# Kernel tuning notes

Measured on AMD Instinct MI355X. Metric: run time of the kernel, lower is better.

The kernel has to match this reference:

```python
import jax, jax.numpy as jnp
import numpy as np

F = 32          # conf['num_features']
G = 96          # voxel grid extent
N_VOX = 80000   # occupied input voxels
BN_EPS = 1e-5


def _encode(c):
    c = c.astype(np.int64) + 8
    return (c[:, 0] * 512 + c[:, 1]) * 512 + c[:, 2]


def _offsets(ks, dil):
    r = np.arange(-(ks // 2), ks // 2 + 1) * dil
    return np.stack(np.meshgrid(r, r, r, indexing='ij'), -1).reshape(-1, 3)


def _build_map(in_coords, out_coords, offsets):
    # For each kernel offset k and output voxel j, find input voxel index at
    # out_coords[j] + offsets[k]; sentinel = n_in / n_out when absent.
    n_in, n_out = len(in_coords), len(out_coords)
    keys = _encode(in_coords)
    order = np.argsort(keys).astype(np.int32)
    skeys = keys[order]
    K = len(offsets)
    in_map = np.full((K, n_out), n_in, np.int32)
    out_map = np.full((K, n_out), n_out, np.int32)
    base = np.arange(n_out, dtype=np.int32)
    for k, off in enumerate(offsets):
        q = _encode(out_coords + off)
        pos = np.clip(np.searchsorted(skeys, q), 0, n_in - 1)
        valid = skeys[pos] == q
        in_map[k] = np.where(valid, order[pos], n_in)
        out_map[k] = np.where(valid, base, n_out)
    return jnp.asarray(in_map), jnp.asarray(out_map)


def setup_inputs() -> dict:
    rng = np.random.default_rng(0)
    idx = rng.choice(G ** 3, size=N_VOX, replace=False)
    coords = np.stack(np.unravel_index(idx, (G, G, G)), 1).astype(np.int64)
    c2 = np.unique(coords // 2 * 2, axis=0)   # stride-2 coords (enc1 output)
    c4 = np.unique(coords // 4 * 4, axis=0)   # stride-4 coords (c_out.C)

    m1_in, m1_out = _build_map(coords, c2, _offsets(5, 1))  # k5 s2 conv
    m2_in, m2_out = _build_map(c2, c2, _offsets(3, 2))      # enc1 blocks
    m3_in, m3_out = _build_map(c2, c4, _offsets(3, 2))      # conv2 -> c_out.C
    m4_in, m4_out = _build_map(c4, c4, _offsets(3, 4))      # enc2 blocks

    key = jax.random.key(0)
    ks = jax.random.split(key, 8)
    s = 0.05
    return {
        'x_geo': jax.random.normal(ks[0], (N_VOX, 1), jnp.float32),
        'x_col': jax.random.uniform(ks[1], (N_VOX, 3), jnp.float32),
        'w0': jax.random.normal(ks[2], (125, 4, F), jnp.float32) * s,
        'w_e1': jax.random.normal(ks[3], (2, 2, 27, F, F), jnp.float32) * s,
        'g_e1': jnp.ones((2, 2, F), jnp.float32),
        'b_e1': jnp.zeros((2, 2, F), jnp.float32),
        'w2': jax.random.normal(ks[4], (27, F, 2 * F), jnp.float32) * s,
        'w_e2': jax.random.normal(ks[5], (2, 2, 27, 2 * F, 2 * F), jnp.float32) * s,
        'g_e2': jnp.ones((2, 2, 2 * F), jnp.float32),
        'b_e2': jnp.zeros((2, 2, 2 * F), jnp.float32),
        'm1_in': m1_in, 'm1_out': m1_out,
        'm2_in': m2_in, 'm2_out': m2_out,
        'm3_in': m3_in, 'm3_out': m3_out,
        'm4_in': m4_in, 'm4_out': m4_out,
    }


def sparse_conv(feats, W, in_map, out_map):
    # gather -> GEMM -> scatter per kernel offset (lax.scan over K offsets)
    n_out = out_map.shape[1]
    fpad = jnp.concatenate([feats, jnp.zeros((1, feats.shape[1]), feats.dtype)], 0)
    out0 = jnp.zeros((n_out + 1, W.shape[2]), feats.dtype)
    def step(acc, kmw):
        im, om, w = kmw
        return acc.at[om].add(fpad[im] @ w), None
    out, _ = jax.lax.scan(step, out0, (in_map, out_map, W))
    return out[:n_out]


def batch_norm(x, g, b):
    mu = x.mean(0)
    var = ((x - mu) ** 2).mean(0)
    return (x - mu) * jax.lax.rsqrt(var + BN_EPS) * g + b


def basic_block(x, w, g, b, in_map, out_map):
    # ME BasicBlock: conv-BN-ReLU-conv-BN + residual, ReLU
    y = jax.nn.relu(batch_norm(sparse_conv(x, w[0], in_map, out_map), g[0], b[0]))
    y = batch_norm(sparse_conv(y, w[1], in_map, out_map), g[1], b[1])
    return jax.nn.relu(y + x)


def reference(x_geo, x_col, w0, w_e1, g_e1, b_e1, w2, w_e2, g_e2, b_e2,
              m1_in, m1_out, m2_in, m2_out, m3_in, m3_out, m4_in, m4_out):
    x = jnp.concatenate([x_geo, x_col], axis=1)          # ME.cat -> 4 channels
    x = jax.nn.relu(sparse_conv(x, w0, m1_in, m1_out))   # k5 s2 conv + ReLU
    for i in range(2):                                   # enc1 residual blocks
        x = basic_block(x, w_e1[i], g_e1[i], b_e1[i], m2_in, m2_out)
    x = sparse_conv(x, w2, m3_in, m3_out)                # conv2 onto c_out.C
    for i in range(2):                                   # enc2 residual blocks
        x = basic_block(x, w_e2[i], g_e2[i], b_e2[i], m4_in, m4_out)
    return x
```

## Files before the change

kernel.cpp:

```cpp
#include <hip/hip_runtime.h>
#include <hip/hip_bf16.h>


typedef float f4 __attribute__((ext_vector_type(4)));
typedef short short8 __attribute__((ext_vector_type(8)));
typedef short short4v __attribute__((ext_vector_type(4)));

#define BN_EPS 1e-5f

static inline int ceil_div(int a, int b) { return (a + b - 1) / b; }

static __device__ inline float btof(short s) {
    unsigned u = ((unsigned)(unsigned short)s) << 16;
    float f;
    __builtin_memcpy(&f, &u, 4);
    return f;
}
static __device__ inline short ftob(float f) {
    __hip_bfloat16 h = __float2bfloat16(f);
    short s;
    __builtin_memcpy(&s, &h, 2);
    return s;
}

struct Seg {
    const float* W;
    long long begin, end;
    int K, CIN, COUT;
};

struct ProArgs {
    Seg s[10];
    const float* geo;
    const float* col;
    __hip_bfloat16* x0;
    int n_vox;
    float* stats;
    __hip_bfloat16* pads[5];
    int padn[5];
    long long wf_total;
    long long pro_total;
    __hip_bfloat16* Wf;
    const int* m1;
    __hip_bfloat16* A;
    int nc2;
};

template <int C>
__device__ inline void bn_coef(const float* st, const float* g, const float* b,
                               int c, int n, float& sc, float& sh) {
    float rn = 1.f / (float)n;
    float sum = st[c] + st[2 * C + c] + st[4 * C + c] + st[6 * C + c];
    float sq  = st[C + c] + st[3 * C + c] + st[5 * C + c] + st[7 * C + c];
    float mu = sum * rn;
    float inv = rsqrtf(sq * rn - mu * mu + BN_EPS);
    sc = inv * g[c];
    sh = b[c] - mu * sc;
}

__global__ __launch_bounds__(256) void k_prologue(ProArgs pa) {
    for (long long e = (long long)blockIdx.x * 256 + threadIdx.x; e < pa.pro_total;
         e += (long long)gridDim.x * 256) {
        if (e < pa.wf_total) {
            int si = 0;
#pragma unroll
            for (int i = 0; i < 10; ++i)
                if (e >= pa.s[i].end) si = i + 1;
            const Seg sg = pa.s[si];
            long long r = e - sg.begin;
            int j = (int)(r & 7);
            int lane = (int)((r >> 3) & 63);
            long long rest = r >> 9;
            int NT = sg.COUT >> 4;
            int ntile = (int)(rest % NT);
            int chunk = (int)(rest / NT);
            int kd = chunk * 32 + ((lane >> 4) << 3) + j;
            int koff = kd / sg.CIN;
            int ci = kd % sg.CIN;
            int n = ntile * 16 + (lane & 15);
            float v = (koff < sg.K) ? sg.W[((size_t)koff * sg.CIN + ci) * sg.COUT + n] : 0.f;
            pa.Wf[e] = __float2bfloat16(v);
            continue;
        }
        long long r = e - pa.wf_total;
        if (r < pa.n_vox) {
            int row = (int)r;
            pa.x0[row * 4 + 0] = __float2bfloat16(pa.geo[row]);
            pa.x0[row * 4 + 1] = __float2bfloat16(pa.col[row * 3 + 0]);
            pa.x0[row * 4 + 2] = __float2bfloat16(pa.col[row * 3 + 1]);
            pa.x0[row * 4 + 3] = __float2bfloat16(pa.col[row * 3 + 2]);
            continue;
        }
        r -= pa.n_vox;
        if (r < 4096) {
            pa.stats[r] = 0.f;
            continue;
        }
        r -= 4096;
#pragma unroll
        for (int i = 0; i < 5; ++i) {
            if (r < pa.padn[i]) {
                pa.pads[i][r] = __float2bfloat16(0.f);
                r = -1;
                break;
            }
            r -= pa.padn[i];
        }
    }
}

__global__ __launch_bounds__(256) void k_stem(ProArgs a) {
    const int t = threadIdx.x, w = t >> 6, lane = t & 63;
    const int quad = lane >> 4, ml = lane & 15;
    const int ntile = w & 1, mgroup = w >> 1;
    const int n_out = a.nc2, n_in = a.n_vox;
    const __hip_bfloat16* feat = a.x0;
    const __hip_bfloat16* Wf = a.Wf;
    const int* in_map = a.m1;
    __hip_bfloat16* out = a.A;
    const int mb = blockIdx.x * 64 + mgroup * 32;
    const int m0 = mb + ml, m1 = mb + 16 + ml;
    const bool v0 = m0 < n_out, v1 = m1 < n_out;
    f4 acc0 = {0.f, 0.f, 0.f, 0.f};
    f4 acc1 = {0.f, 0.f, 0.f, 0.f};
#pragma unroll 2
    for (int chunk = 0; chunk < 16; ++chunk) {
        int k0 = chunk * 8 + quad * 2;
        int k1 = k0 + 1;
        int k0c = (k0 < 125) ? k0 : 0;
        int k1c = (k1 < 125) ? k1 : 0;
        short8 b = *(const short8*)(Wf + ((size_t)(chunk * 2 + ntile) * 64 + lane) * 8);
        int ia = v0 ? in_map[(size_t)k0c * n_out + m0] : n_in;
        int ib = v0 ? in_map[(size_t)k1c * n_out + m0] : n_in;
        int ic = v1 ? in_map[(size_t)k0c * n_out + m1] : n_in;
        int id = v1 ? in_map[(size_t)k1c * n_out + m1] : n_in;
        short4v p0 = *(const short4v*)(feat + (size_t)ia * 4);
        short4v p1 = *(const short4v*)(feat + (size_t)ib * 4);
        short4v p2 = *(const short4v*)(feat + (size_t)ic * 4);
        short4v p3 = *(const short4v*)(feat + (size_t)id * 4);
        short8 a0, a1;
        a0[0] = p0[0]; a0[1] = p0[1]; a0[2] = p0[2]; a0[3] = p0[3];
        a0[4] = p1[0]; a0[5] = p1[1]; a0[6] = p1[2]; a0[7] = p1[3];
        a1[0] = p2[0]; a1[1] = p2[1]; a1[2] = p2[2]; a1[3] = p2[3];
        a1[4] = p3[0]; a1[5] = p3[1]; a1[6] = p3[2]; a1[7] = p3[3];
        acc0 = __builtin_amdgcn_mfma_f32_16x16x32_bf16(a0, b, acc0, 0, 0, 0);
        acc1 = __builtin_amdgcn_mfma_f32_16x16x32_bf16(a1, b, acc1, 0, 0, 0);
    }
    const int col = ntile * 16 + ml;
#pragma unroll
    for (int i = 0; i < 4; ++i) {
        int r0 = mb + quad * 4 + i;
        if (r0 < n_out)
            out[(size_t)r0 * 32 + col] = __float2bfloat16(fmaxf(acc0[i], 0.f));
        int r1 = mb + 16 + quad * 4 + i;
        if (r1 < n_out)
            out[(size_t)r1 * 32 + col] = __float2bfloat16(fmaxf(acc1[i], 0.f));
    }
}

template <int CIN, int COUT, int MT, int K, bool BNF>
__global__ __launch_bounds__(256, 4) void k_conv(
    const __hip_bfloat16* __restrict__ feat,
    const __hip_bfloat16* __restrict__ Wf,
    const int* __restrict__ in_map,
    __hip_bfloat16* __restrict__ out,
    float* __restrict__ stats,
    const float* __restrict__ in_stats,
    const float* __restrict__ in_g,
    const float* __restrict__ in_b,
    int n_out, int n_in) {
    constexpr int NT = COUT / 16;
    constexpr int H = CIN / 32;
    constexpr int R = MT * 16;
    constexpr int KPW = (K + 3) / 4;
    constexpr int SP = COUT + 1;
    const int t = threadIdx.x, w = t >> 6, lane = t & 63;
    const int quad = lane >> 4, ml = lane & 15;
    const int mb = blockIdx.x * R;

    __shared__ float red[4 * R * SP];
    __shared__ float sred[2 * 256];
    __shared__ float ibn[2 * CIN];

    if constexpr (BNF) {
        if (t < CIN) {
            float sc, sh;
            bn_coef<CIN>(in_stats, in_g, in_b, t, n_in, sc, sh);
            ibn[t] = sc;
            ibn[CIN + t] = sh;
        }
        __syncthreads();
    }
    float scr[H][8], shr[H][8];
    if constexpr (BNF) {
#pragma unroll
        for (int h = 0; h < H; ++h)
#pragma unroll
            for (int j = 0; j < 8; ++j) {
                int ch = h * 32 + quad * 8 + j;
                scr[h][j] = ibn[ch];
                shr[h][j] = ibn[CIN + ch];
            }
    }

    f4 acc[MT * NT];
#pragma unroll
    for (int i = 0; i < MT * NT; ++i) acc[i] = (f4){0.f, 0.f, 0.f, 0.f};

#pragma unroll
    for (int kk = 0; kk < KPW; ++kk) {
        const int k = kk * 4 + w;
        const int krow = (k < K) ? k : 0;
        const int* mk = in_map + (size_t)krow * n_out;
        int idx[MT];
#pragma unroll
        for (int mi = 0; mi < MT; ++mi) {
            int m = mb + mi * 16 + ml;
            idx[mi] = (m < n_out) ? mk[m] : n_in;
        }
        short8 bfrag[H * NT];
#pragma unroll
        for (int h = 0; h < H; ++h)
#pragma unroll
            for (int nt = 0; nt < NT; ++nt)
                bfrag[h * NT + nt] = *(const short8*)(
                    Wf + (((size_t)(k * H + h) * NT + nt) * 64 + lane) * 8);
#pragma unroll
        for (int mi = 0; mi < MT; ++mi) {
            const __hip_bfloat16* fp = feat + (size_t)idx[mi] * CIN + quad * 8;
            const bool sent = (idx[mi] == n_in);
#pragma unroll
            for (int h = 0; h < H; ++h) {
                short8 av = *(const short8*)(fp + h * 32);
                if constexpr (BNF) {
#pragma unroll
                    for (int j = 0; j < 8; ++j) {
                        float f = btof(av[j]) * scr[h][j] + shr[h][j];
                        f = fmaxf(f, 0.f);
                        av[j] = sent ? (short)0 : ftob(f);
                    }
                }
#pragma unroll
                for (int nt = 0; nt < NT; ++nt)
                    acc[mi * NT + nt] = __builtin_amdgcn_mfma_f32_16x16x32_bf16(
                        av, bfrag[h * NT + nt], acc[mi * NT + nt], 0, 0, 0);
            }
        }
    }

#pragma unroll
    for (int mi = 0; mi < MT; ++mi)
#pragma unroll
        for (int nt = 0; nt < NT; ++nt)
#pragma unroll
            for (int i = 0; i < 4; ++i)
                red[((size_t)w * R + mi * 16 + quad * 4 + i) * SP + nt * 16 + ml] =
                    acc[mi * NT + nt][i];
    __syncthreads();

    constexpr int E = (R * COUT) / 256;
    constexpr int RSTEP = 256 / COUT;
    const int col = t % COUT;
    const int rg = t / COUT;
    float s = 0.f, s2 = 0.f;
#pragma unroll
    for (int i = 0; i < E; ++i) {
        int r = rg + i * RSTEP;
        float v = red[(0 * R + r) * SP + col] + red[(1 * R + r) * SP + col] +
                  red[(2 * R + r) * SP + col] + red[(3 * R + r) * SP + col];
        s += v;
        s2 += v * v;
        int grow = mb + r;
        if (grow < n_out) out[(size_t)grow * COUT + col] = __float2bfloat16(v);
    }

    if (stats) {
        sred[t] = s;
        sred[256 + t] = s2;
        __syncthreads();
        if (t < 2 * COUT) {
            int c = t % COUT;
            int which = t / COUT;
            float v = 0.f;
#pragma unroll
            for (int j = 0; j < RSTEP; ++j) v += sred[which * 256 + j * COUT + c];
            atomicAdd(&stats[((blockIdx.x & 3) * 2 + which) * COUT + c], v);
        }
    }
}

template <int C, bool F32OUT>
__global__ __launch_bounds__(256) void k_bnres(
    const __hip_bfloat16* __restrict__ y, const __hip_bfloat16* __restrict__ res,
    const float* __restrict__ st, const float* __restrict__ g,
    const float* __restrict__ b, void* outp, int n) {
    __shared__ float ibn[2 * C];
    const int t = threadIdx.x;
    if (t < C) {
        float sc, sh;
        bn_coef<C>(st, g, b, t, n, sc, sh);
        ibn[t] = sc;
        ibn[C + t] = sh;
    }
    __syncthreads();
    long long tot = (long long)n * (C / 8);
    long long i = (long long)blockIdx.x * 256 + t;
    if (i >= tot) return;
    int c0 = (int)(i % (C / 8)) * 8;
    short8 v = *(const short8*)(y + i * 8);
    short8 r = *(const short8*)(res + i * 8);
    if constexpr (F32OUT) {
        float* out = (float*)outp;
        f4 o0, o1;
#pragma unroll
        for (int j = 0; j < 8; ++j) {
            float f = btof(v[j]) * ibn[c0 + j] + ibn[C + c0 + j] + btof(r[j]);
            f = fmaxf(f, 0.f);
            if (j < 4) o0[j] = f; else o1[j - 4] = f;
        }
        *(f4*)(out + i * 8) = o0;
        *(f4*)(out + i * 8 + 4) = o1;
    } else {
        __hip_bfloat16* out = (__hip_bfloat16*)outp;
        short8 o;
#pragma unroll
        for (int j = 0; j < 8; ++j) {
            float f = btof(v[j]) * ibn[c0 + j] + ibn[C + c0 + j] + btof(r[j]);
            o[j] = ftob(fmaxf(f, 0.f));
        }
        *(short8*)(out + i * 8) = o;
    }
}

extern "C" void kernel_launch(void* const* d_in, const int* in_sizes, int n_in_cnt,
                              void* d_out, int out_size, void* d_ws, size_t ws_size,
                              hipStream_t stream) {
    const float* x_geo = (const float*)d_in[0];
    const float* x_col = (const float*)d_in[1];
    const float* w0    = (const float*)d_in[2];
    const float* w_e1  = (const float*)d_in[3];
    const float* g_e1  = (const float*)d_in[4];
    const float* b_e1  = (const float*)d_in[5];
    const float* w2    = (const float*)d_in[6];
    const float* w_e2  = (const float*)d_in[7];
    const float* g_e2  = (const float*)d_in[8];
    const float* b_e2  = (const float*)d_in[9];
    const int* m1 = (const int*)d_in[10];
    const int* m2 = (const int*)d_in[12];
    const int* m3 = (const int*)d_in[14];
    const int* m4 = (const int*)d_in[16];

    const int n_vox = in_sizes[0];
    const int nc2 = in_sizes[10] / 125;
    const int nc4 = in_sizes[14] / 27;
    (void)out_size; (void)ws_size; (void)n_in_cnt;

    char* p = (char*)d_ws;
    auto alloc = [&](size_t bytes) -> char* {
        char* r = p;
        p += (bytes + 255) & ~(size_t)255;
        return r;
    };
    float* stats = (float*)alloc(8 * 512 * sizeof(float));
    __hip_bfloat16* x0 = (__hip_bfloat16*)alloc((size_t)(n_vox + 1) * 4 * 2);
    __hip_bfloat16* A  = (__hip_bfloat16*)alloc((size_t)(nc2 + 1) * 32 * 2);
    __hip_bfloat16* B  = (__hip_bfloat16*)alloc((size_t)(nc2 + 1) * 32 * 2);
    __hip_bfloat16* Cb = (__hip_bfloat16*)alloc((size_t)(nc2 + 1) * 32 * 2);
    __hip_bfloat16* D  = (__hip_bfloat16*)alloc((size_t)(nc4 + 1) * 64 * 2);
    __hip_bfloat16* E  = (__hip_bfloat16*)alloc((size_t)(nc4 + 1) * 64 * 2);
    __hip_bfloat16* Fb = (__hip_bfloat16*)alloc((size_t)(nc4 + 1) * 64 * 2);

    const long long sz_stem = 16LL * 2 * 512;
    const long long sz_e1   = 28LL * 2 * 512;
    const long long sz_c2   = 28LL * 4 * 512;
    const long long sz_e2   = 56LL * 4 * 512;
    const long long wf_total = sz_stem + 4 * sz_e1 + sz_c2 + 4 * sz_e2;
    __hip_bfloat16* Wf = (__hip_bfloat16*)alloc((size_t)wf_total * 2);

    ProArgs pa;
    long long cur = 0;
    auto seg = [&](int i, const float* W, int K, int CIN, int COUT, long long n) {
        pa.s[i].W = W; pa.s[i].K = K; pa.s[i].CIN = CIN; pa.s[i].COUT = COUT;
        pa.s[i].begin = cur; pa.s[i].end = cur + n; cur += n;
    };
    seg(0, w0, 125, 4, 32, sz_stem);
    for (int i = 0; i < 4; ++i)
        seg(1 + i, w_e1 + (size_t)i * 27 * 32 * 32, 27, 32, 32, sz_e1);
    seg(5, w2, 27, 32, 64, sz_c2);
    for (int i = 0; i < 4; ++i)
        seg(6 + i, w_e2 + (size_t)i * 27 * 64 * 64, 27, 64, 64, sz_e2);

    long long off_e1[4], off_e2[4];
    cur = sz_stem;
    for (int i = 0; i < 4; ++i) { off_e1[i] = cur; cur += sz_e1; }
    long long off_c2 = cur; cur += sz_c2;
    for (int i = 0; i < 4; ++i) { off_e2[i] = cur; cur += sz_e2; }

    pa.geo = x_geo; pa.col = x_col; pa.x0 = x0; pa.n_vox = n_vox;
    pa.stats = stats;
    pa.pads[0] = x0 + (size_t)n_vox * 4; pa.padn[0] = 4;
    pa.pads[1] = A + (size_t)nc2 * 32;   pa.padn[1] = 32;
    pa.pads[2] = B + (size_t)nc2 * 32;   pa.padn[2] = 32;
    pa.pads[3] = D + (size_t)nc4 * 64;   pa.padn[3] = 64;
    pa.pads[4] = E + (size_t)nc4 * 64;   pa.padn[4] = 64;
    pa.wf_total = wf_total;
    pa.pro_total = wf_total + n_vox + 4096 + (4 + 32 + 32 + 64 + 64);
    pa.Wf = Wf;
    pa.m1 = m1;
    pa.A = A;
    pa.nc2 = nc2;

    k_prologue<<<ceil_div((int)pa.pro_total, 256), 256, 0, stream>>>(pa);
    k_stem<<<ceil_div(nc2, 64), 256, 0, stream>>>(pa);

    k_conv<32, 32, 4, 27, false><<<ceil_div(nc2, 64), 256, 0, stream>>>(
        A, Wf + off_e1[0], m2, B, stats + 0 * 512,
        nullptr, nullptr, nullptr, nc2, nc2);
    k_conv<32, 32, 4, 27, true><<<ceil_div(nc2, 64), 256, 0, stream>>>(
        B, Wf + off_e1[1], m2, Cb, stats + 1 * 512,
        stats + 0 * 512, g_e1 + 0, b_e1 + 0, nc2, nc2);
    k_bnres<32, false><<<ceil_div(nc2 * 4, 256), 256, 0, stream>>>(
        Cb, A, stats + 1 * 512, g_e1 + 32, b_e1 + 32, A, nc2);

    k_conv<32, 32, 4, 27, false><<<ceil_div(nc2, 64), 256, 0, stream>>>(
        A, Wf + off_e1[2], m2, B, stats + 2 * 512,
        nullptr, nullptr, nullptr, nc2, nc2);
    k_conv<32, 32, 4, 27, true><<<ceil_div(nc2, 64), 256, 0, stream>>>(
        B, Wf + off_e1[3], m2, Cb, stats + 3 * 512,
        stats + 2 * 512, g_e1 + 64, b_e1 + 64, nc2, nc2);
    k_bnres<32, false><<<ceil_div(nc2 * 4, 256), 256, 0, stream>>>(
        Cb, A, stats + 3 * 512, g_e1 + 96, b_e1 + 96, A, nc2);

    k_conv<32, 64, 1, 27, false><<<ceil_div(nc4, 16), 256, 0, stream>>>(
        A, Wf + off_c2, m3, D, nullptr,
        nullptr, nullptr, nullptr, nc4, nc2);

    k_conv<64, 64, 1, 27, false><<<ceil_div(nc4, 16), 256, 0, stream>>>(
        D, Wf + off_e2[0], m4, E, stats + 4 * 512,
        nullptr, nullptr, nullptr, nc4, nc4);
    k_conv<64, 64, 1, 27, true><<<ceil_div(nc4, 16), 256, 0, stream>>>(
        E, Wf + off_e2[1], m4, Fb, stats + 5 * 512,
        stats + 4 * 512, g_e2 + 0, b_e2 + 0, nc4, nc4);
    k_bnres<64, false><<<ceil_div(nc4 * 8, 256), 256, 0, stream>>>(
        Fb, D, stats + 5 * 512, g_e2 + 64, b_e2 + 64, D, nc4);

    k_conv<64, 64, 1, 27, false><<<ceil_div(nc4, 16), 256, 0, stream>>>(
        D, Wf + off_e2[2], m4, E, stats + 6 * 512,
        nullptr, nullptr, nullptr, nc4, nc4);
    k_conv<64, 64, 1, 27, true><<<ceil_div(nc4, 16), 256, 0, stream>>>(
        E, Wf + off_e2[3], m4, Fb, stats + 7 * 512,
        stats + 6 * 512, g_e2 + 128, b_e2 + 128, nc4, nc4);
    k_bnres<64, true><<<ceil_div(nc4 * 8, 256), 256, 0, stream>>>(
        Fb, D, stats + 7 * 512, g_e2 + 192, b_e2 + 192, (float*)d_out, nc4);
}
```

Baseline: 321.4 us.

## Unfuse BN-ReLU from gather conv and split kernel offsets across more waves

```diff
diff --git a/kernel.cpp b/kernel.cpp
--- a/kernel.cpp
+++ b/kernel.cpp
@@ -158,92 +158,58 @@
     }
 }
 
-template <int CIN, int COUT, int MT, int K, bool BNF>
-__global__ __launch_bounds__(256, 4) void k_conv(
+template <int CIN, int COUT, int MT, int K, int SPLIT>
+__global__ __launch_bounds__(64 * SPLIT, (SPLIT) == 8 ? 6 : 4) void k_conv(
     const __hip_bfloat16* __restrict__ feat,
     const __hip_bfloat16* __restrict__ Wf,
     const int* __restrict__ in_map,
     __hip_bfloat16* __restrict__ out,
     float* __restrict__ stats,
-    const float* __restrict__ in_stats,
-    const float* __restrict__ in_g,
-    const float* __restrict__ in_b,
     int n_out, int n_in) {
     constexpr int NT = COUT / 16;
     constexpr int H = CIN / 32;
     constexpr int R = MT * 16;
-    constexpr int KPW = (K + 3) / 4;
-    constexpr int SP = COUT + 1;
+    constexpr int KPW = (K + SPLIT - 1) / SPLIT;
+    constexpr int SP = COUT + 4;
+    constexpr int BS = 64 * SPLIT;
     const int t = threadIdx.x, w = t >> 6, lane = t & 63;
     const int quad = lane >> 4, ml = lane & 15;
     const int mb = blockIdx.x * R;
 
-    __shared__ float red[4 * R * SP];
-    __shared__ float sred[2 * 256];
-    __shared__ float ibn[2 * CIN];
-
-    if constexpr (BNF) {
-        if (t < CIN) {
-            float sc, sh;
-            bn_coef<CIN>(in_stats, in_g, in_b, t, n_in, sc, sh);
-            ibn[t] = sc;
-            ibn[CIN + t] = sh;
-        }
-        __syncthreads();
-    }
-    float scr[H][8], shr[H][8];
-    if constexpr (BNF) {
-#pragma unroll
-        for (int h = 0; h < H; ++h)
-#pragma unroll
-            for (int j = 0; j < 8; ++j) {
-                int ch = h * 32 + quad * 8 + j;
-                scr[h][j] = ibn[ch];
-                shr[h][j] = ibn[CIN + ch];
+    __shared__ float red[SPLIT * R * SP];
+    __shared__ float sred[2 * BS];
+
+    f4 acc[MT * NT];
+#pragma unroll
+    for (int i = 0; i < MT * NT; ++i) acc[i] = (f4){0.f, 0.f, 0.f, 0.f};
+
+#pragma unroll
+    for (int kk = 0; kk < KPW; ++kk) {
+        const int k = kk * SPLIT + w;
+        if (k < K) {
+            const int* mk = in_map + (size_t)k * n_out;
+            int idx[MT];
+#pragma unroll
+            for (int mi = 0; mi < MT; ++mi) {
+                int m = mb + mi * 16 + ml;
+                idx[mi] = (m < n_out) ? mk[m] : n_in;
             }
-    }
-
-    f4 acc[MT * NT];
-#pragma unroll
-    for (int i = 0; i < MT * NT; ++i) acc[i] = (f4){0.f, 0.f, 0.f, 0.f};
-
-#pragma unroll
-    for (int kk = 0; kk < KPW; ++kk) {
-        const int k = kk * 4 + w;
-        const int krow = (k < K) ? k : 0;
-        const int* mk = in_map + (size_t)krow * n_out;
-        int idx[MT];
-#pragma unroll
-        for (int mi = 0; mi < MT; ++mi) {
-            int m = mb + mi * 16 + ml;
-            idx[mi] = (m < n_out) ? mk[m] : n_in;
-        }
-        short8 bfrag[H * NT];
-#pragma unroll
-        for (int h = 0; h < H; ++h)
-#pragma unroll
-            for (int nt = 0; nt < NT; ++nt)
-                bfrag[h * NT + nt] = *(const short8*)(
-                    Wf + (((size_t)(k * H + h) * NT + nt) * 64 + lane) * 8);
-#pragma unroll
-        for (int mi = 0; mi < MT; ++mi) {
-            const __hip_bfloat16* fp = feat + (size_t)idx[mi] * CIN + quad * 8;
-            const bool sent = (idx[mi] == n_in);
 #pragma unroll
             for (int h = 0; h < H; ++h) {
-                short8 av = *(const short8*)(fp + h * 32);
-                if constexpr (BNF) {
-#pragma unroll
-                    for (int j = 0; j < 8; ++j) {
-                        float f = btof(av[j]) * scr[h][j] + shr[h][j];
-                        f = fmaxf(f, 0.f);
-                        av[j] = sent ? (short)0 : ftob(f);
-                    }
+                short8 bfrag[NT];
+#pragma unroll
+                for (int nt = 0; nt < NT; ++nt)
+                    bfrag[nt] = *(const short8*)(
+                        Wf + (((size_t)(k * H + h) * NT + nt) * 64 + lane) * 8);
+#pragma unroll
+                for (int mi = 0; mi < MT; ++mi) {
+                    short8 av = *(const short8*)(
+                        feat + (size_t)idx[mi] * CIN + h * 32 + quad * 8);
+#pragma unroll
+                    for (int nt = 0; nt < NT; ++nt)
+                        acc[mi * NT + nt] = __builtin_amdgcn_mfma_f32_16x16x32_bf16(
+                            av, bfrag[nt], acc[mi * NT + nt], 0, 0, 0);
                 }
-#pragma unroll
-                for (int nt = 0; nt < NT; ++nt)
-                    acc[mi * NT + nt] = __builtin_amdgcn_mfma_f32_16x16x32_bf16(
-                        av, bfrag[h * NT + nt], acc[mi * NT + nt], 0, 0, 0);
             }
         }
     }
@@ -254,20 +220,21 @@
         for (int nt = 0; nt < NT; ++nt)
 #pragma unroll
             for (int i = 0; i < 4; ++i)
-                red[((size_t)w * R + mi * 16 + quad * 4 + i) * SP + nt * 16 + ml] =
+                red[(w * R + mi * 16 + quad * 4 + i) * SP + nt * 16 + ml] =
                     acc[mi * NT + nt][i];
     __syncthreads();
 
-    constexpr int E = (R * COUT) / 256;
-    constexpr int RSTEP = 256 / COUT;
+    constexpr int E = (R * COUT) / BS;
+    constexpr int RSTEP = BS / COUT;
     const int col = t % COUT;
     const int rg = t / COUT;
     float s = 0.f, s2 = 0.f;
 #pragma unroll
     for (int i = 0; i < E; ++i) {
         int r = rg + i * RSTEP;
-        float v = red[(0 * R + r) * SP + col] + red[(1 * R + r) * SP + col] +
-                  red[(2 * R + r) * SP + col] + red[(3 * R + r) * SP + col];
+        float v = 0.f;
+#pragma unroll
+        for (int sp = 0; sp < SPLIT; ++sp) v += red[(sp * R + r) * SP + col];
         s += v;
         s2 += v * v;
         int grow = mb + r;
@@ -276,17 +243,44 @@
 
     if (stats) {
         sred[t] = s;
-        sred[256 + t] = s2;
+        sred[BS + t] = s2;
         __syncthreads();
         if (t < 2 * COUT) {
             int c = t % COUT;
             int which = t / COUT;
             float v = 0.f;
 #pragma unroll
-            for (int j = 0; j < RSTEP; ++j) v += sred[which * 256 + j * COUT + c];
+            for (int j = 0; j < RSTEP; ++j) v += sred[which * BS + j * COUT + c];
             atomicAdd(&stats[((blockIdx.x & 3) * 2 + which) * COUT + c], v);
         }
     }
+}
+
+template <int C>
+__global__ __launch_bounds__(256) void k_bnact(
+    __hip_bfloat16* __restrict__ x, const float* __restrict__ st,
+    const float* __restrict__ g, const float* __restrict__ b, int n) {
+    __shared__ float ibn[2 * C];
+    const int t = threadIdx.x;
+    if (t < C) {
+        float sc, sh;
+        bn_coef<C>(st, g, b, t, n, sc, sh);
+        ibn[t] = sc;
+        ibn[C + t] = sh;
+    }
+    __syncthreads();
+    long long tot = (long long)n * (C / 8);
+    long long i = (long long)blockIdx.x * 256 + t;
+    if (i >= tot) return;
+    int c0 = (int)(i % (C / 8)) * 8;
+    short8 v = *(const short8*)(x + i * 8);
+    short8 o;
+#pragma unroll
+    for (int j = 0; j < 8; ++j) {
+        float f = btof(v[j]) * ibn[c0 + j] + ibn[C + c0 + j];
+        o[j] = ftob(fmaxf(f, 0.f));
+    }
+    *(short8*)(x + i * 8) = o;
 }
 
 template <int C, bool F32OUT>
@@ -372,8 +366,8 @@
 
     const long long sz_stem = 16LL * 2 * 512;
     const long long sz_e1   = 28LL * 2 * 512;
-    const long long sz_c2   = 28LL * 4 * 512;
-    const long long sz_e2   = 56LL * 4 * 512;
+    const long long sz_c2   = 32LL * 4 * 512;
+    const long long sz_e2   = 32LL * 8 * 512;
     const long long wf_total = sz_stem + 4 * sz_e1 + sz_c2 + 4 * sz_e2;
     __hip_bfloat16* Wf = (__hip_bfloat16*)alloc((size_t)wf_total * 2);
 
@@ -413,43 +407,42 @@
     k_prologue<<<ceil_div((int)pa.pro_total, 256), 256, 0, stream>>>(pa);
     k_stem<<<ceil_div(nc2, 64), 256, 0, stream>>>(pa);
 
-    k_conv<32, 32, 4, 27, false><<<ceil_div(nc2, 64), 256, 0, stream>>>(
-        A, Wf + off_e1[0], m2, B, stats + 0 * 512,
-        nullptr, nullptr, nullptr, nc2, nc2);
-    k_conv<32, 32, 4, 27, true><<<ceil_div(nc2, 64), 256, 0, stream>>>(
-        B, Wf + off_e1[1], m2, Cb, stats + 1 * 512,
-        stats + 0 * 512, g_e1 + 0, b_e1 + 0, nc2, nc2);
+    k_conv<32, 32, 2, 27, 4><<<ceil_div(nc2, 32), 256, 0, stream>>>(
+        A, Wf + off_e1[0], m2, B, stats + 0 * 512, nc2, nc2);
+    k_bnact<32><<<ceil_div(nc2 * 4, 256), 256, 0, stream>>>(
+        B, stats + 0 * 512, g_e1 + 0, b_e1 + 0, nc2);
+    k_conv<32, 32, 2, 27, 4><<<ceil_div(nc2, 32), 256, 0, stream>>>(
+        B, Wf + off_e1[1], m2, Cb, stats + 1 * 512, nc2, nc2);
     k_bnres<32, false><<<ceil_div(nc2 * 4, 256), 256, 0, stream>>>(
         Cb, A, stats + 1 * 512, g_e1 + 32, b_e1 + 32, A, nc2);
 
-    k_conv<32, 32, 4, 27, false><<<ceil_div(nc2, 64), 256, 0, stream>>>(
-        A, Wf + off_e1[2], m2, B, stats + 2 * 512,
-        nullptr, nullptr, nullptr, nc2, nc2);
-    k_conv<32, 32, 4, 27, true><<<ceil_div(nc2, 64), 256, 0, stream>>>(
-        B, Wf + off_e1[3], m2, Cb, stats + 3 * 512,
-        stats + 2 * 512, g_e1 + 64, b_e1 + 64, nc2, nc2);
+    k_conv<32, 32, 2, 27, 4><<<ceil_div(nc2, 32), 256, 0, stream>>>(
+        A, Wf + off_e1[2], m2, B, stats + 2 * 512, nc2, nc2);
+    k_bnact<32><<<ceil_div(nc2 * 4, 256), 256, 0, stream>>>(
+        B, stats + 2 * 512, g_e1 + 64, b_e1 + 64, nc2);
+    k_conv<32, 32, 2, 27, 4><<<ceil_div(nc2, 32), 256, 0, stream>>>(
+        B, Wf + off_e1[3], m2, Cb, stats + 3 * 512, nc2, nc2);
     k_bnres<32, false><<<ceil_div(nc2 * 4, 256), 256, 0, stream>>>(
         Cb, A, stats + 3 * 512, g_e1 + 96, b_e1 + 96, A, nc2);
 
-    k_conv<32, 64, 1, 27, false><<<ceil_div(nc4, 16), 256, 0, stream>>>(
-        A, Wf + off_c2, m3, D, nullptr,
-        nullptr, nullptr, nullptr, nc4, nc2);
-
-    k_conv<64, 64, 1, 27, false><<<ceil_div(nc4, 16), 256, 0, stream>>>(
-        D, Wf + off_e2[0], m4, E, stats + 4 * 512,
-        nullptr, nullptr, nullptr, nc4, nc4);
-    k_conv<64, 64, 1, 27, true><<<ceil_div(nc4, 16), 256, 0, stream>>>(
-        E, Wf + off_e2[1], m4, Fb, stats + 5 * 512,
-        stats + 4 * 512, g_e2 + 0, b_e2 + 0, nc4, nc4);
+    k_conv<32, 64, 1, 27, 8><<<ceil_div(nc4, 16), 512, 0, stream>>>(
+        A, Wf + off_c2, m3, D, nullptr, nc4, nc2);
+
+    k_conv<64, 64, 1, 27, 8><<<ceil_div(nc4, 16), 512, 0, stream>>>(
+        D, Wf + off_e2[0], m4, E, stats + 4 * 512, nc4, nc4);
+    k_bnact<64><<<ceil_div(nc4 * 8, 256), 256, 0, stream>>>(
+        E, stats + 4 * 512, g_e2 + 0, b_e2 + 0, nc4);
+    k_conv<64, 64, 1, 27, 8><<<ceil_div(nc4, 16), 512, 0, stream>>>(
+        E, Wf + off_e2[1], m4, Fb, stats + 5 * 512, nc4, nc4);
     k_bnres<64, false><<<ceil_div(nc4 * 8, 256), 256, 0, stream>>>(
         Fb, D, stats + 5 * 512, g_e2 + 64, b_e2 + 64, D, nc4);
 
-    k_conv<64, 64, 1, 27, false><<<ceil_div(nc4, 16), 256, 0, stream>>>(
-        D, Wf + off_e2[2], m4, E, stats + 6 * 512,
-        nullptr, nullptr, nullptr, nc4, nc4);
-    k_conv<64, 64, 1, 27, true><<<ceil_div(nc4, 16), 256, 0, stream>>>(
-        E, Wf + off_e2[3], m4, Fb, stats + 7 * 512,
-        stats + 6 * 512, g_e2 + 128, b_e2 + 128, nc4, nc4);
+    k_conv<64, 64, 1, 27, 8><<<ceil_div(nc4, 16), 512, 0, stream>>>(
+        D, Wf + off_e2[2], m4, E, stats + 6 * 512, nc4, nc4);
+    k_bnact<64><<<ceil_div(nc4 * 8, 256), 256, 0, stream>>>(
+        E, stats + 6 * 512, g_e2 + 128, b_e2 + 128, nc4);
+    k_conv<64, 64, 1, 27, 8><<<ceil_div(nc4, 16), 512, 0, stream>>>(
+        E, Wf + off_e2[3], m4, Fb, stats + 7 * 512, nc4, nc4);
     k_bnres<64, true><<<ceil_div(nc4 * 8, 256), 256, 0, stream>>>(
         Fb, D, stats + 7 * 512, g_e2 + 192, b_e2 + 192, (float*)d_out, nc4);
 }
```

Result: slower. 349.5 us (+8.7%).

## Add register-only sparse conv kernel for enc1 residual blocks

Applied to the files above, without the earlier changes.

```diff
diff --git a/kernel.cpp b/kernel.cpp
--- a/kernel.cpp
+++ b/kernel.cpp
@@ -51,7 +51,9 @@
                                int c, int n, float& sc, float& sh) {
     float rn = 1.f / (float)n;
     float sum = st[c] + st[2 * C + c] + st[4 * C + c] + st[6 * C + c];
-    float sq  = st[C + c] + st[3 * C + c] + st[5 * C + c] + st[7 * C + c];
+    float sq  = st[C + c] + st[3 * C + c] + st[5 * C + c] + st[6 * C + c] -
+                st[6 * C + c] + st[7 * C + c] - st[3 * C + c] + st[3 * C + c];
+    sq = st[C + c] + st[3 * C + c] + st[5 * C + c] + st[7 * C + c];
     float mu = sum * rn;
     float inv = rsqrtf(sq * rn - mu * mu + BN_EPS);
     sc = inv * g[c];
@@ -158,6 +160,99 @@
     }
 }
 
+template <int CIN, int COUT, int K, bool BNF>
+__global__ __launch_bounds__(256, 4) void k_convm(
+    const __hip_bfloat16* __restrict__ feat,
+    const __hip_bfloat16* __restrict__ Wf,
+    const int* __restrict__ in_map,
+    __hip_bfloat16* __restrict__ out,
+    float* __restrict__ stats,
+    const float* __restrict__ in_stats,
+    const float* __restrict__ in_g,
+    const float* __restrict__ in_b,
+    int n_out, int n_in) {
+    constexpr int NT = COUT / 16;
+    constexpr int H = CIN / 32;
+    const int t = threadIdx.x, w = t >> 6, lane = t & 63;
+    const int quad = lane >> 4, ml = lane & 15;
+    const int rb = blockIdx.x * 64 + w * 16;
+
+    float scr[H][8], shr[H][8];
+    if constexpr (BNF) {
+#pragma unroll
+        for (int h = 0; h < H; ++h)
+#pragma unroll
+            for (int j = 0; j < 8; ++j) {
+                int ch = h * 32 + quad * 8 + j;
+                bn_coef<CIN>(in_stats, in_g, in_b, ch, n_in, scr[h][j], shr[h][j]);
+            }
+    }
+
+    f4 acc[NT];
+#pragma unroll
+    for (int i = 0; i < NT; ++i) acc[i] = (f4){0.f, 0.f, 0.f, 0.f};
+
+    const int m = rb + ml;
+    const bool mv = m < n_out;
+
+#pragma unroll
+    for (int k = 0; k < K; ++k) {
+        int idx = mv ? in_map[(size_t)k * n_out + m] : n_in;
+        const __hip_bfloat16* fp = feat + (size_t)idx * CIN + quad * 8;
+        const bool sent = (idx == n_in);
+#pragma unroll
+        for (int h = 0; h < H; ++h) {
+            short8 av = *(const short8*)(fp + h * 32);
+            if constexpr (BNF) {
+#pragma unroll
+                for (int j = 0; j < 8; ++j) {
+                    float f = btof(av[j]) * scr[h][j] + shr[h][j];
+                    f = fmaxf(f, 0.f);
+                    av[j] = sent ? (short)0 : ftob(f);
+                }
+            }
+#pragma unroll
+            for (int nt = 0; nt < NT; ++nt) {
+                short8 bfrag = *(const short8*)(
+                    Wf + (((size_t)(k * H + h) * NT + nt) * 64 + lane) * 8);
+                acc[nt] = __builtin_amdgcn_mfma_f32_16x16x32_bf16(
+                    av, bfrag, acc[nt], 0, 0, 0);
+            }
+        }
+    }
+
+#pragma unroll
+    for (int nt = 0; nt < NT; ++nt)
+#pragma unroll
+        for (int i = 0; i < 4; ++i) {
+            int row = rb + quad * 4 + i;
+            if (row < n_out)
+                out[(size_t)row * COUT + nt * 16 + ml] = __float2bfloat16(acc[nt][i]);
+        }
+
+    if (stats) {
+        const int slot = blockIdx.x & 3;
+#pragma unroll
+        for (int nt = 0; nt < NT; ++nt) {
+            float s = 0.f, s2 = 0.f;
+#pragma unroll
+            for (int i = 0; i < 4; ++i) {
+                float v = acc[nt][i];
+                s += v;
+                s2 += v * v;
+            }
+            s += __shfl_xor(s, 16);
+            s += __shfl_xor(s, 32);
+            s2 += __shfl_xor(s2, 16);
+            s2 += __shfl_xor(s2, 32);
+            if (quad == 0)
+                atomicAdd(&stats[(slot * 2 + 0) * COUT + nt * 16 + ml], s);
+            if (quad == 1)
+                atomicAdd(&stats[(slot * 2 + 1) * COUT + nt * 16 + ml], s2);
+        }
+    }
+}
+
 template <int CIN, int COUT, int MT, int K, bool BNF>
 __global__ __launch_bounds__(256, 4) void k_conv(
     const __hip_bfloat16* __restrict__ feat,
@@ -413,19 +508,19 @@
     k_prologue<<<ceil_div((int)pa.pro_total, 256), 256, 0, stream>>>(pa);
     k_stem<<<ceil_div(nc2, 64), 256, 0, stream>>>(pa);
 
-    k_conv<32, 32, 4, 27, false><<<ceil_div(nc2, 64), 256, 0, stream>>>(
+    k_convm<32, 32, 27, false><<<ceil_div(nc2, 64), 256, 0, stream>>>(
         A, Wf + off_e1[0], m2, B, stats + 0 * 512,
         nullptr, nullptr, nullptr, nc2, nc2);
-    k_conv<32, 32, 4, 27, true><<<ceil_div(nc2, 64), 256, 0, stream>>>(
+    k_convm<32, 32, 27, true><<<ceil_div(nc2, 64), 256, 0, stream>>>(
         B, Wf + off_e1[1], m2, Cb, stats + 1 * 512,
         stats + 0 * 512, g_e1 + 0, b_e1 + 0, nc2, nc2);
     k_bnres<32, false><<<ceil_div(nc2 * 4, 256), 256, 0, stream>>>(
         Cb, A, stats + 1 * 512, g_e1 + 32, b_e1 + 32, A, nc2);
 
-    k_conv<32, 32, 4, 27, false><<<ceil_div(nc2, 64), 256, 0, stream>>>(
+    k_convm<32, 32, 27, false><<<ceil_div(nc2, 64), 256, 0, stream>>>(
         A, Wf + off_e1[2], m2, B, stats + 2 * 512,
         nullptr, nullptr, nullptr, nc2, nc2);
-    k_conv<32, 32, 4, 27, true><<<ceil_div(nc2, 64), 256, 0, stream>>>(
+    k_convm<32, 32, 27, true><<<ceil_div(nc2, 64), 256, 0, stream>>>(
         B, Wf + off_e1[3], m2, Cb, stats + 3 * 512,
         stats + 2 * 512, g_e1 + 64, b_e1 + 64, nc2, nc2);
     k_bnres<32, false><<<ceil_div(nc2 * 4, 256), 256, 0, stream>>>(
```

Measured after the change: 421.5 us. +31.1%, slower.
